# Optimization experiments

Hardware: AMD Instinct MI355X
Metric: run time of the kernel (lower is better)

## Reference

```python
import jax, jax.numpy as jnp
import numpy as np

N_NODES = 10000
N_EDGES = 100000
N_GRAPHS = 64
EMBED = 512
HIDDEN = 1024
N_LAYERS = 3
N_GAUSS = 50
RBF_RADIUS = 12.0
AVG_LEN = 60.0
CONNECTIVITY = 32.0


def setup_inputs() -> dict:
    key = jax.random.key(0)
    ks = jax.random.split(key, 20)
    x = jax.random.normal(ks[0], (N_NODES, EMBED), dtype=jnp.float32)
    edge_index = jax.random.randint(ks[1], (2, N_EDGES), 0, N_NODES, dtype=jnp.int32)
    batch = jnp.sort(jax.random.randint(ks[2], (N_NODES,), 0, N_GRAPHS, dtype=jnp.int32))
    dist = jax.random.uniform(ks[3], (N_EDGES,), dtype=jnp.float32) * RBF_RADIUS
    v = jax.random.normal(ks[4], (N_EDGES, 3), dtype=jnp.float32)
    vec_hat = v / (jnp.linalg.norm(v, axis=-1, keepdims=True) + 1e-12)

    def lin(k, fan_in, shape):
        bound = 1.0 / np.sqrt(fan_in)
        return jax.random.uniform(k, shape, jnp.float32, -bound, bound)

    in_dim = 3 * EMBED
    params = {
        'rbf_W': lin(ks[5], N_GAUSS, (N_GAUSS, EMBED)),
        'rbf_b': lin(ks[6], N_GAUSS, (EMBED,)),
        'e_Win': lin(ks[7], in_dim, (in_dim, HIDDEN)),
        'e_bin': lin(ks[8], in_dim, (HIDDEN,)),
        'e_Wh': lin(ks[9], HIDDEN, (N_LAYERS, HIDDEN, HIDDEN)),
        'e_bh': lin(ks[10], HIDDEN, (N_LAYERS, HIDDEN)),
        'e_Wout': lin(ks[11], HIDDEN, (HIDDEN, 1)),
        'e_bout': lin(ks[12], HIDDEN, (1,)),
        'f_Win': lin(ks[13], in_dim, (in_dim, HIDDEN)),
        'f_bin': lin(ks[14], in_dim, (HIDDEN,)),
        'f_Wh': lin(ks[15], HIDDEN, (N_LAYERS, HIDDEN, HIDDEN)),
        'f_bh': lin(ks[16], HIDDEN, (N_LAYERS, HIDDEN)),
        'f_Wout': lin(ks[17], HIDDEN, (HIDDEN, 1)),
        'f_bout': lin(ks[18], HIDDEN, (1,)),
    }
    return {'x': x, 'edge_index': edge_index, 'batch': batch, 'dist': dist,
            'vec_hat': vec_hat, **params}


def _rbf(dist, W, b):
    # Gaussian smearing over [0, rbf_radius] followed by linear embed
    offsets = jnp.linspace(0.0, RBF_RADIUS, N_GAUSS, dtype=jnp.float32)
    coeff = -0.5 / (offsets[1] - offsets[0]) ** 2
    gauss = jnp.exp(coeff * (dist[:, None] - offsets[None, :]) ** 2)  # [E, G]
    return gauss @ W + b  # [E, embed]


def _resmlp(h, Win, bin_, Wh, bh, Wout, bout):
    h = jax.nn.silu(h @ Win + bin_)
    for i in range(N_LAYERS):
        h = h + jax.nn.silu(h @ Wh[i] + bh[i])
    return h @ Wout + bout  # [E, 1]


def reference(x, edge_index, batch, dist, vec_hat,
              rbf_W, rbf_b,
              e_Win, e_bin, e_Wh, e_bh, e_Wout, e_bout,
              f_Win, f_bin, f_Wh, f_bh, f_Wout, f_bout):
    src, dst = edge_index[0], edge_index[1]
    rbf = _rbf(dist, rbf_W, rbf_b)  # [E, embed]
    inputs = jnp.concatenate([x[src], x[dst], rbf], axis=-1)  # [E, 3*embed]
    energy_pairs = _resmlp(inputs, e_Win, e_bin, e_Wh, e_bh, e_Wout, e_bout)  # [E,1]
    force_pairs = _resmlp(inputs, f_Win, f_bin, f_Wh, f_bh, f_Wout, f_bout) * vec_hat  # [E,3]
    energy = jax.ops.segment_sum(energy_pairs, batch[src], num_segments=N_GRAPHS)
    energy = energy / (AVG_LEN * CONNECTIVITY)  # [G,1]
    forces = jax.ops.segment_sum(force_pairs, src, num_segments=N_NODES) / CONNECTIVITY  # [N,3]
    return energy, forces
```

## Files before the change

kernel.cpp:

```cpp
#include <hip/hip_runtime.h>

#define E_EDGES 100000
#define E_PAD   100096
#define NNODES  10000
#define NPAD    10112
#define NGRAPHS 64

typedef __attribute__((ext_vector_type(4))) float f32x4;
typedef __attribute__((ext_vector_type(8))) short short8;

__device__ __forceinline__ unsigned short f2bf(float f) {
  union { float f; unsigned u; } v; v.f = f;
  unsigned u = v.u;
  return (unsigned short)((u + 0x7FFFu + ((u >> 16) & 1u)) >> 16);
}
__device__ __forceinline__ float bf2f(unsigned short h) {
  union { unsigned u; float f; } v; v.u = ((unsigned)h) << 16;
  return v.f;
}

struct TDesc { const float* src; unsigned short* dst; int R, C, srcLd, dstLd; };
struct TDescs { TDesc d[10]; };

__global__ __launch_bounds__(256) void transpose_all(TDescs ds) {
  TDesc t = ds.d[blockIdx.z];
  int x0 = blockIdx.x * 32, y0 = blockIdx.y * 32;
  if (x0 >= t.C || y0 >= t.R) return;
  __shared__ float tile[32][33];
  int tx = threadIdx.x & 31, ty = threadIdx.x >> 5;
#pragma unroll
  for (int i = 0; i < 4; ++i)
    tile[ty + i * 8][tx] = t.src[(size_t)(y0 + ty + i * 8) * t.srcLd + x0 + tx];
  __syncthreads();
#pragma unroll
  for (int i = 0; i < 4; ++i) {
    int c = ty + i * 8;
    t.dst[(size_t)(x0 + c) * t.dstLd + y0 + tx] = f2bf(tile[tx][c]);
  }
}

__global__ void mbuild_kernel(const float* __restrict__ rbf_W, const float* __restrict__ rbf_b,
                              const float* __restrict__ e_Win, const float* __restrict__ e_bin,
                              const float* __restrict__ f_Win, const float* __restrict__ f_bin,
                              unsigned short* __restrict__ M_t) {
  int gid = blockIdx.x * 256 + threadIdx.x;
  int n = gid >> 6, k = gid & 63;
  const float* Wp; float bn; int col;
  if (n < 1024) { Wp = e_Win + 1024 * 1024; col = n;        bn = e_bin[n]; }
  else          { Wp = f_Win + 1024 * 1024; col = n - 1024; bn = f_bin[n - 1024]; }
  float acc = 0.f;
  if (k < 50) {
    for (int i = 0; i < 512; ++i) acc += rbf_W[k * 512 + i] * Wp[(size_t)i * 1024 + col];
  } else if (k == 50) {
    for (int i = 0; i < 512; ++i) acc += rbf_b[i] * Wp[(size_t)i * 1024 + col];
    acc += bn;
  }
  M_t[n * 64 + k] = f2bf(acc);
}

__global__ void gauss_kernel(const float* __restrict__ dist, unsigned short* __restrict__ G) {
  int gid = blockIdx.x * 256 + threadIdx.x;
  if (gid >= E_PAD * 64) return;
  int e = gid >> 6, g = gid & 63;
  float val = 0.f;
  if (e < E_EDGES) {
    if (g < 50) {
      const float step = 12.0f / 49.0f;
      float d = dist[e] - step * (float)g;
      val = __expf((-0.5f / (step * step)) * d * d);
    } else if (g == 50) val = 1.0f;
  }
  G[gid] = f2bf(val);
}

__global__ void xconv_kernel(const float* __restrict__ x, unsigned short* __restrict__ xb) {
  int gid = blockIdx.x * 256 + threadIdx.x;
  int r = gid >> 9;
  xb[gid] = f2bf(r < NNODES ? x[gid] : 0.f);
}

template<int MODE>
__global__ __launch_bounds__(256, 3)
void gemm_kernel(const unsigned short* __restrict__ A, const unsigned short* __restrict__ Bt,
                 const float* __restrict__ bias, unsigned short* __restrict__ C,
                 const float* __restrict__ wout, float* __restrict__ pairs,
                 int K, int ldc, int nRows, int nColBlk) {
  __shared__ __align__(16) unsigned short As[128 * 64];
  __shared__ __align__(16) unsigned short Bs[128 * 64];
  const int nblk = gridDim.x;
  const int bid  = blockIdx.x;
  const int swz  = (bid & 7) * (nblk >> 3) + (bid >> 3);
  const int rowBlk = swz / nColBlk;
  const int colBlk = swz - rowBlk * nColBlk;
  const int rowBase = rowBlk * 128;
  const int colBase = colBlk * 128;
  const int tid  = threadIdx.x;
  const int wave = tid >> 6, lane = tid & 63;
  const int wr = wave >> 1, wc = wave & 1;
  const int lrow = lane & 15;
  const int lk   = (lane >> 4) << 3;
  const int r0 = (lane >> 4) << 2;
  const int c0 = lane & 15;
  const int ktRes = (colBase >> 6) + wc;

  f32x4 acc[4][4];
#pragma unroll
  for (int m = 0; m < 4; ++m)
#pragma unroll
    for (int n = 0; n < 4; ++n) acc[m][n] = (f32x4){0.f, 0.f, 0.f, 0.f};

  unsigned short resv[4][4][4];

  const int nk = K >> 6;
  for (int kt = 0; kt < nk; ++kt) {
    const int k0 = kt << 6;
    __syncthreads();
#pragma unroll
    for (int i = 0; i < 4; ++i) {
      int chunk = wave * 4 + i;
      int eoff  = (chunk * 64 + lane) * 8;
      int r = eoff >> 6, c = eoff & 63;
      const unsigned short* ga = A  + (size_t)(rowBase + r) * K + (k0 + c);
      const unsigned short* gb = Bt + (size_t)(colBase + r) * K + (k0 + c);
      __builtin_amdgcn_global_load_lds((const __attribute__((address_space(1))) void*)ga,
          (__attribute__((address_space(3))) void*)(As + chunk * 512), 16, 0, 0);
      __builtin_amdgcn_global_load_lds((const __attribute__((address_space(1))) void*)gb,
          (__attribute__((address_space(3))) void*)(Bs + chunk * 512), 16, 0, 0);
    }
    __syncthreads();
#pragma unroll
    for (int kk = 0; kk < 2; ++kk) {
      short8 a[4], b[4];
#pragma unroll
      for (int m = 0; m < 4; ++m)
        a[m] = *(const short8*)&As[(wr * 64 + m * 16 + lrow) * 64 + kk * 32 + lk];
#pragma unroll
      for (int n = 0; n < 4; ++n)
        b[n] = *(const short8*)&Bs[(wc * 64 + n * 16 + lrow) * 64 + kk * 32 + lk];
#pragma unroll
      for (int m = 0; m < 4; ++m)
#pragma unroll
        for (int n = 0; n < 4; ++n)
          acc[m][n] = __builtin_amdgcn_mfma_f32_16x16x32_bf16(a[m], b[n], acc[m][n], 0, 0, 0);
    }
    if (MODE >= 1 && kt == ktRes) {
#pragma unroll
      for (int m = 0; m < 4; ++m)
#pragma unroll
        for (int n = 0; n < 4; ++n)
#pragma unroll
          for (int j = 0; j < 4; ++j)
            resv[m][n][j] = As[(wr * 64 + m * 16 + r0 + j) * 64 + (n * 16 + c0)];
    }
  }

  float rsum[4][4];
  if (MODE == 2) {
#pragma unroll
    for (int m = 0; m < 4; ++m)
#pragma unroll
      for (int j = 0; j < 4; ++j) rsum[m][j] = 0.f;
  }

#pragma unroll
  for (int n = 0; n < 4; ++n) {
    int colg = colBase + wc * 64 + n * 16 + c0;
    float bv = (MODE >= 1) ? bias[colg] : 0.f;
    float wv = (MODE == 2) ? wout[colg] : 0.f;
#pragma unroll
    for (int m = 0; m < 4; ++m) {
      int rowg = rowBase + wr * 64 + m * 16 + r0;
#pragma unroll
      for (int j = 0; j < 4; ++j) {
        float v = acc[m][n][j] + bv;
        float s;
        if (MODE >= 1) s = v / (1.f + __expf(-v)) + bf2f(resv[m][n][j]);
        else           s = v;
        if (MODE == 2) rsum[m][j] += s * wv;
        else           C[(size_t)(rowg + j) * ldc + colg] = f2bf(s);
      }
    }
  }

  if (MODE == 2) {
#pragma unroll
    for (int m = 0; m < 4; ++m)
#pragma unroll
      for (int j = 0; j < 4; ++j) {
        float v = rsum[m][j];
        v += __shfl_xor(v, 1); v += __shfl_xor(v, 2);
        v += __shfl_xor(v, 4); v += __shfl_xor(v, 8);
        if (c0 == 0) {
          int rowg = rowBase + wr * 64 + m * 16 + r0 + j;
          if (rowg < nRows) atomicAdd(&pairs[rowg], v);
        }
      }
  }
}

__global__ __launch_bounds__(256, 3)
void fuse1_kernel(const unsigned short* __restrict__ G, const unsigned short* __restrict__ M_t,
                  const unsigned short* __restrict__ PS, const int* __restrict__ srcI,
                  const int* __restrict__ dstI, unsigned short* __restrict__ H,
                  int colOff, int e0) {
  __shared__ __align__(16) unsigned short Gs[128 * 64];
  __shared__ __align__(16) unsigned short Ms[128 * 64];
  __shared__ int sIdx[128], dIdx[128];
  const int rowBase = blockIdx.x * 128;
  const int nBase   = blockIdx.y * 128;
  const int tid  = threadIdx.x;
  const int wave = tid >> 6, lane = tid & 63;
  const int wr = wave >> 1, wc = wave & 1;
  const int lrow = lane & 15;
  const int lk   = (lane >> 4) << 3;

  {
    int r = tid & 127;
    int e = e0 + rowBase + r;
    if (tid < 128) sIdx[r] = (e < E_EDGES) ? srcI[e] : 0;
    else           dIdx[r] = (e < E_EDGES) ? dstI[e] : 0;
  }
#pragma unroll
  for (int i = 0; i < 4; ++i) {
    int chunk = wave * 4 + i;
    int eoff  = (chunk * 64 + lane) * 8;
    const unsigned short* gg = G   + (size_t)(e0 + rowBase) * 64 + eoff;
    const unsigned short* gm = M_t + (size_t)(colOff + nBase) * 64 + eoff;
    __builtin_amdgcn_global_load_lds((const __attribute__((address_space(1))) void*)gg,
        (__attribute__((address_space(3))) void*)(Gs + chunk * 512), 16, 0, 0);
    __builtin_amdgcn_global_load_lds((const __attribute__((address_space(1))) void*)gm,
        (__attribute__((address_space(3))) void*)(Ms + chunk * 512), 16, 0, 0);
  }
  __syncthreads();

  f32x4 acc[4][4];
#pragma unroll
  for (int m = 0; m < 4; ++m)
#pragma unroll
    for (int n = 0; n < 4; ++n) acc[m][n] = (f32x4){0.f, 0.f, 0.f, 0.f};
#pragma unroll
  for (int kk = 0; kk < 2; ++kk) {
    short8 a[4], b[4];
#pragma unroll
    for (int m = 0; m < 4; ++m)
      a[m] = *(const short8*)&Gs[(wr * 64 + m * 16 + lrow) * 64 + kk * 32 + lk];
#pragma unroll
    for (int n = 0; n < 4; ++n)
      b[n] = *(const short8*)&Ms[(wc * 64 + n * 16 + lrow) * 64 + kk * 32 + lk];
#pragma unroll
    for (int m = 0; m < 4; ++m)
#pragma unroll
      for (int n = 0; n < 4; ++n)
        acc[m][n] = __builtin_amdgcn_mfma_f32_16x16x32_bf16(a[m], b[n], acc[m][n], 0, 0, 0);
  }

  const int r0 = (lane >> 4) << 2;
  const int c0 = lane & 15;
#pragma unroll
  for (int m = 0; m < 4; ++m)
#pragma unroll
    for (int j = 0; j < 4; ++j) {
      int rowl = wr * 64 + m * 16 + r0 + j;
      int s = sIdx[rowl], d = dIdx[rowl];
      const unsigned short* prs = PS + (size_t)s * 4096 + 2 * colOff;
      const unsigned short* prd = PS + (size_t)d * 4096 + 2 * colOff + 1024;
#pragma unroll
      for (int n = 0; n < 4; ++n) {
        int nloc = nBase + wc * 64 + n * 16 + c0;
        float v = acc[m][n][j] + bf2f(prs[nloc]) + bf2f(prd[nloc]);
        H[(size_t)(rowBase + rowl) * 1024 + nloc] = f2bf(v / (1.f + __expf(-v)));
      }
    }
}

__global__ void init_kernel(float* __restrict__ pe, float* __restrict__ pf,
                            float* __restrict__ out, int outN,
                            const float* __restrict__ eb, const float* __restrict__ fb) {
  int i = blockIdx.x * 256 + threadIdx.x;
  if (i < E_EDGES) pe[i] = eb[0];
  else if (i < 2 * E_EDGES) pf[i - E_EDGES] = fb[0];
  else if (i < 2 * E_EDGES + outN) out[i - 2 * E_EDGES] = 0.f;
}

__global__ void energy_kernel(const float* __restrict__ pairs, const int* __restrict__ srcI,
                              const int* __restrict__ batch, float* __restrict__ out) {
  __shared__ float bins[NGRAPHS];
  if (threadIdx.x < NGRAPHS) bins[threadIdx.x] = 0.f;
  __syncthreads();
  for (int e = blockIdx.x * 256 + threadIdx.x; e < E_EDGES; e += gridDim.x * 256)
    atomicAdd(&bins[batch[srcI[e]]], pairs[e]);
  __syncthreads();
  if (threadIdx.x < NGRAPHS)
    atomicAdd(&out[threadIdx.x], bins[threadIdx.x] * (1.0f / 1920.0f));
}

__global__ void force_kernel(const float* __restrict__ pairs, const int* __restrict__ srcI,
                             const float* __restrict__ vec, float* __restrict__ out) {
  int e = blockIdx.x * 256 + threadIdx.x;
  if (e >= E_EDGES) return;
  float p = pairs[e] * (1.0f / 32.0f);
  int s = srcI[e];
  atomicAdd(&out[64 + s * 3 + 0], p * vec[e * 3 + 0]);
  atomicAdd(&out[64 + s * 3 + 1], p * vec[e * 3 + 1]);
  atomicAdd(&out[64 + s * 3 + 2], p * vec[e * 3 + 2]);
}

extern "C" void kernel_launch(void* const* d_in, const int* in_sizes, int n_in,
                              void* d_out, int out_size, void* d_ws, size_t ws_size,
                              hipStream_t stream) {
  const float* x       = (const float*)d_in[0];
  const int*   ei      = (const int*)  d_in[1];
  const int*   batch   = (const int*)  d_in[2];
  const float* dist    = (const float*)d_in[3];
  const float* vec_hat = (const float*)d_in[4];
  const float* rbf_W   = (const float*)d_in[5];
  const float* rbf_b   = (const float*)d_in[6];
  const float* e_Win   = (const float*)d_in[7];
  const float* e_bin   = (const float*)d_in[8];
  const float* e_Wh    = (const float*)d_in[9];
  const float* e_bh    = (const float*)d_in[10];
  const float* e_Wout  = (const float*)d_in[11];
  const float* e_bout  = (const float*)d_in[12];
  const float* f_Win   = (const float*)d_in[13];
  const float* f_bin   = (const float*)d_in[14];
  const float* f_Wh    = (const float*)d_in[15];
  const float* f_bh    = (const float*)d_in[16];
  const float* f_Wout  = (const float*)d_in[17];
  const float* f_bout  = (const float*)d_in[18];

  const int* srcI = ei;
  const int* dstI = ei + E_EDGES;

  size_t off = 0;
  char* base = (char*)d_ws;
  auto alloc = [&](size_t bytes) -> void* {
    void* p = base + off;
    off = (off + bytes + 255) & ~(size_t)255;
    return p;
  };
  unsigned short* WtN   = (unsigned short*)alloc((size_t)4096 * 512 * 2);
  unsigned short* Wt_eh = (unsigned short*)alloc((size_t)3 * 1024 * 1024 * 2);
  unsigned short* Wt_fh = (unsigned short*)alloc((size_t)3 * 1024 * 1024 * 2);
  unsigned short* M_t   = (unsigned short*)alloc((size_t)2048 * 64 * 2);
  unsigned short* xb    = (unsigned short*)alloc((size_t)NPAD * 512 * 2);
  unsigned short* G     = (unsigned short*)alloc((size_t)E_PAD * 64 * 2);
  unsigned short* PS    = (unsigned short*)alloc((size_t)NPAD * 4096 * 2);
  float* pairs_e = (float*)alloc((size_t)E_EDGES * 4);
  float* pairs_f = (float*)alloc((size_t)E_EDGES * 4);

  size_t avail = (ws_size > off + 4096) ? (ws_size - off - 4096) : 0;
  long long rows = (long long)(avail / 4096);
  int EC = (int)(rows - rows % 128);
  if (EC > E_PAD) EC = E_PAD;
  if (EC < 128) return;

  unsigned short* bufA = (unsigned short*)alloc((size_t)EC * 1024 * 2);
  unsigned short* bufC = (unsigned short*)alloc((size_t)EC * 1024 * 2);
  if (ws_size < off) return;

  init_kernel<<<(2 * E_EDGES + out_size + 255) / 256, 256, 0, stream>>>(
      pairs_e, pairs_f, (float*)d_out, out_size, e_bout, f_bout);

  TDescs td;
  td.d[0] = {e_Win,              WtN,               512, 1024, 1024, 512};
  td.d[1] = {e_Win + 512 * 1024, WtN + 1024 * 512,  512, 1024, 1024, 512};
  td.d[2] = {f_Win,              WtN + 2048 * 512,  512, 1024, 1024, 512};
  td.d[3] = {f_Win + 512 * 1024, WtN + 3072 * 512,  512, 1024, 1024, 512};
  for (int l = 0; l < 3; ++l) {
    td.d[4 + l] = {e_Wh + (size_t)l * 1048576, Wt_eh + (size_t)l * 1048576, 1024, 1024, 1024, 1024};
    td.d[7 + l] = {f_Wh + (size_t)l * 1048576, Wt_fh + (size_t)l * 1048576, 1024, 1024, 1024, 1024};
  }
  transpose_all<<<dim3(32, 32, 10), 256, 0, stream>>>(td);

  mbuild_kernel<<<(2048 * 64) / 256, 256, 0, stream>>>(rbf_W, rbf_b, e_Win, e_bin, f_Win, f_bin, M_t);
  gauss_kernel<<<(E_PAD * 64) / 256, 256, 0, stream>>>(dist, G);
  xconv_kernel<<<(NPAD * 512) / 256, 256, 0, stream>>>(x, xb);

  gemm_kernel<0><<<(NPAD / 128) * 32, 256, 0, stream>>>(
      xb, WtN, nullptr, PS, nullptr, nullptr, 512, 4096, NPAD, 32);

  for (int e0 = 0; e0 < E_EDGES; e0 += EC) {
    int rem = E_EDGES - e0; if (rem > EC) rem = EC;
    int rowsPad = ((rem + 127) / 128) * 128;
    int nblk = (rowsPad / 128) * 8;
    dim3 gf(rowsPad / 128, 8);

    fuse1_kernel<<<gf, 256, 0, stream>>>(G, M_t, PS, srcI, dstI, bufA, 0, e0);
    gemm_kernel<1><<<nblk, 256, 0, stream>>>(bufA, Wt_eh + (size_t)0 * 1048576, e_bh + 0,
                                             bufC, nullptr, nullptr, 1024, 1024, rowsPad, 8);
    gemm_kernel<1><<<nblk, 256, 0, stream>>>(bufC, Wt_eh + (size_t)1 * 1048576, e_bh + 1024,
                                             bufA, nullptr, nullptr, 1024, 1024, rowsPad, 8);
    gemm_kernel<2><<<nblk, 256, 0, stream>>>(bufA, Wt_eh + (size_t)2 * 1048576, e_bh + 2048,
                                             nullptr, e_Wout, pairs_e + e0, 1024, 1024, rem, 8);

    fuse1_kernel<<<gf, 256, 0, stream>>>(G, M_t, PS, srcI, dstI, bufC, 1024, e0);
    gemm_kernel<1><<<nblk, 256, 0, stream>>>(bufC, Wt_fh + (size_t)0 * 1048576, f_bh + 0,
                                             bufA, nullptr, nullptr, 1024, 1024, rowsPad, 8);
    gemm_kernel<1><<<nblk, 256, 0, stream>>>(bufA, Wt_fh + (size_t)1 * 1048576, f_bh + 1024,
                                             bufC, nullptr, nullptr, 1024, 1024, rowsPad, 8);
    gemm_kernel<2><<<nblk, 256, 0, stream>>>(bufC, Wt_fh + (size_t)2 * 1048576, f_bh + 2048,
                                             nullptr, f_Wout, pairs_f + e0, 1024, 1024, rem, 8);
  }

  energy_kernel<<<256, 256, 0, stream>>>(pairs_e, srcI, batch, (float*)d_out);
  force_kernel<<<(E_EDGES + 255) / 256, 256, 0, stream>>>(pairs_f, srcI, vec_hat, (float*)d_out);
}
```

Measured before the change: 2.225 ms.

## Replace hidden-layer GEMMs with 256x256 tile, double-buffered, 8-wave pipelined kernel

Adds a gemm8_kernel that computes 256x256 output tiles with 8 waves, a double-buffered 128KB LDS stage, an XOR swizzle against bank conflicts, interleaved global-to-LDS prefetch with split MFMA phases, s_setprio, and an XCD-aware block remap. The residual is now read from global memory in the epilogue instead of being captured from LDS. The old gemm kernel is reduced to the plain MODE 0 projection. The aim is more operand reuse per tile and overlap of loads with MFMA in the dominant 1024x1024 layers. In exchange it uses large LDS that limits occupancy, pads edges to 256 rows, and adds an extra global read for the residual.

```diff
diff --git a/kernel.cpp b/kernel.cpp
--- a/kernel.cpp
+++ b/kernel.cpp
@@ -101,15 +101,12 @@
   const int lk   = (lane >> 4) << 3;
   const int r0 = (lane >> 4) << 2;
   const int c0 = lane & 15;
-  const int ktRes = (colBase >> 6) + wc;
 
   f32x4 acc[4][4];
 #pragma unroll
   for (int m = 0; m < 4; ++m)
 #pragma unroll
     for (int n = 0; n < 4; ++n) acc[m][n] = (f32x4){0.f, 0.f, 0.f, 0.f};
-
-  unsigned short resv[4][4][4];
 
   const int nk = K >> 6;
   for (int kt = 0; kt < nk; ++kt) {
@@ -143,55 +140,178 @@
         for (int n = 0; n < 4; ++n)
           acc[m][n] = __builtin_amdgcn_mfma_f32_16x16x32_bf16(a[m], b[n], acc[m][n], 0, 0, 0);
     }
-    if (MODE >= 1 && kt == ktRes) {
-#pragma unroll
-      for (int m = 0; m < 4; ++m)
-#pragma unroll
-        for (int n = 0; n < 4; ++n)
-#pragma unroll
-          for (int j = 0; j < 4; ++j)
-            resv[m][n][j] = As[(wr * 64 + m * 16 + r0 + j) * 64 + (n * 16 + c0)];
-    }
-  }
-
-  float rsum[4][4];
-  if (MODE == 2) {
-#pragma unroll
-    for (int m = 0; m < 4; ++m)
-#pragma unroll
-      for (int j = 0; j < 4; ++j) rsum[m][j] = 0.f;
   }
 
 #pragma unroll
   for (int n = 0; n < 4; ++n) {
     int colg = colBase + wc * 64 + n * 16 + c0;
-    float bv = (MODE >= 1) ? bias[colg] : 0.f;
-    float wv = (MODE == 2) ? wout[colg] : 0.f;
 #pragma unroll
     for (int m = 0; m < 4; ++m) {
       int rowg = rowBase + wr * 64 + m * 16 + r0;
 #pragma unroll
+      for (int j = 0; j < 4; ++j)
+        C[(size_t)(rowg + j) * ldc + colg] = f2bf(acc[m][n][j]);
+    }
+  }
+}
+
+template<int MODE>
+__global__ __launch_bounds__(512, 2)
+void gemm8_kernel(const unsigned short* __restrict__ A, const unsigned short* __restrict__ Bt,
+                  const float* __restrict__ bias, unsigned short* __restrict__ C,
+                  const float* __restrict__ wout, float* __restrict__ pairs,
+                  int K, int nRows, int nColBlk) {
+  __shared__ __align__(16) char smem[131072];
+  const int nwg = gridDim.x, orig = blockIdx.x;
+  const int xcd = orig & 7, q = nwg >> 3, rr = nwg & 7;
+  const int wgid = (xcd < rr ? xcd * (q + 1) : rr * (q + 1) + (xcd - rr) * q) + (orig >> 3);
+  const int rowBlk = wgid / nColBlk;
+  const int colBlk = wgid - rowBlk * nColBlk;
+  const int rowBase = rowBlk * 256, colBase = colBlk * 256;
+  const int tid = threadIdx.x, w = tid >> 6, lane = tid & 63;
+  const int wr = w >> 2, wcn = w & 3;
+  const int lrow = lane & 15, hi = lane >> 4;
+  const int r0 = hi << 2, c0 = lane & 15;
+  const int nk = K >> 6;
+
+  auto stageHalf = [&](const unsigned short* gsrc, char* ldsBase) {
+#pragma unroll
+    for (int i = 0; i < 2; ++i) {
+      int r = i * 64 + w * 8 + (lane >> 3);
+      int cb = ((lane & 7) * 16) ^ (((r >> 2) & 1) << 6);
+      __builtin_amdgcn_global_load_lds(
+          (const __attribute__((address_space(1))) void*)(gsrc + (size_t)r * K + (cb >> 1)),
+          (__attribute__((address_space(3))) void*)(ldsBase + i * 8192 + w * 1024), 16, 0, 0);
+    }
+  };
+  auto stageA = [&](int t, int h) {
+    stageHalf(A + (size_t)(rowBase + h * 128) * K + t * 64, smem + (t & 1) * 65536 + h * 16384);
+  };
+  auto stageB = [&](int t, int h) {
+    stageHalf(Bt + (size_t)(colBase + h * 128) * K + t * 64,
+              smem + (t & 1) * 65536 + 32768 + h * 16384);
+  };
+  auto ldsA = [&](int c, int m, int ks) -> short8 {
+    const char* hb = smem + c * 65536 + wr * 16384;
+    int row = m * 16 + lrow;
+    int byte = ((row << 7) | (ks * 64 + hi * 16)) ^ (((row >> 2) & 1) << 6);
+    return *(const short8*)(hb + byte);
+  };
+  auto ldsB = [&](int c, int n, int ks) -> short8 {
+    const char* hb = smem + c * 65536 + 32768 + (wcn >> 1) * 16384;
+    int row = (wcn & 1) * 64 + n * 16 + lrow;
+    int byte = ((row << 7) | (ks * 64 + hi * 16)) ^ (((row >> 2) & 1) << 6);
+    return *(const short8*)(hb + byte);
+  };
+
+  f32x4 acc[8][4];
+#pragma unroll
+  for (int m = 0; m < 8; ++m)
+#pragma unroll
+    for (int n = 0; n < 4; ++n) acc[m][n] = (f32x4){0.f, 0.f, 0.f, 0.f};
+  short8 aF[8][2], bF[2][2];
+
+  stageA(0, 0); stageA(0, 1); stageB(0, 0); stageB(0, 1);
+  stageA(1, 0); stageA(1, 1);
+  asm volatile("s_waitcnt vmcnt(4)" ::: "memory");
+  asm volatile("s_barrier" ::: "memory");
+
+  for (int t = 0; t < nk; ++t) {
+    const int c = t & 1;
+    if (t + 1 < nk) stageB(t + 1, 0);
+#pragma unroll
+    for (int m = 0; m < 4; ++m) { aF[m][0] = ldsA(c, m, 0); aF[m][1] = ldsA(c, m, 1); }
+#pragma unroll
+    for (int n = 0; n < 2; ++n) { bF[n][0] = ldsB(c, n, 0); bF[n][1] = ldsB(c, n, 1); }
+    asm volatile("s_barrier" ::: "memory");
+    __builtin_amdgcn_s_setprio(1);
+#pragma unroll
+    for (int m = 0; m < 4; ++m)
+#pragma unroll
+      for (int n = 0; n < 2; ++n)
+#pragma unroll
+        for (int ks = 0; ks < 2; ++ks)
+          acc[m][n] = __builtin_amdgcn_mfma_f32_16x16x32_bf16(aF[m][ks], bF[n][ks], acc[m][n], 0, 0, 0);
+    __builtin_amdgcn_s_setprio(0);
+    asm volatile("s_barrier" ::: "memory");
+    if (t + 1 < nk) stageB(t + 1, 1);
+#pragma unroll
+    for (int m = 4; m < 8; ++m) { aF[m][0] = ldsA(c, m, 0); aF[m][1] = ldsA(c, m, 1); }
+    asm volatile("s_barrier" ::: "memory");
+    __builtin_amdgcn_s_setprio(1);
+#pragma unroll
+    for (int m = 4; m < 8; ++m)
+#pragma unroll
+      for (int n = 0; n < 2; ++n)
+#pragma unroll
+        for (int ks = 0; ks < 2; ++ks)
+          acc[m][n] = __builtin_amdgcn_mfma_f32_16x16x32_bf16(aF[m][ks], bF[n][ks], acc[m][n], 0, 0, 0);
+    __builtin_amdgcn_s_setprio(0);
+    asm volatile("s_barrier" ::: "memory");
+    if (t + 2 < nk) stageA(t + 2, 0);
+#pragma unroll
+    for (int n = 0; n < 2; ++n) { bF[n][0] = ldsB(c, n + 2, 0); bF[n][1] = ldsB(c, n + 2, 1); }
+    asm volatile("s_barrier" ::: "memory");
+    __builtin_amdgcn_s_setprio(1);
+#pragma unroll
+    for (int m = 4; m < 8; ++m)
+#pragma unroll
+      for (int n = 0; n < 2; ++n)
+#pragma unroll
+        for (int ks = 0; ks < 2; ++ks)
+          acc[m][n + 2] = __builtin_amdgcn_mfma_f32_16x16x32_bf16(aF[m][ks], bF[n][ks], acc[m][n + 2], 0, 0, 0);
+    __builtin_amdgcn_s_setprio(0);
+    asm volatile("s_barrier" ::: "memory");
+    if (t + 2 < nk) stageA(t + 2, 1);
+    asm volatile("s_barrier" ::: "memory");
+    __builtin_amdgcn_s_setprio(1);
+#pragma unroll
+    for (int m = 0; m < 4; ++m)
+#pragma unroll
+      for (int n = 0; n < 2; ++n)
+#pragma unroll
+        for (int ks = 0; ks < 2; ++ks)
+          acc[m][n + 2] = __builtin_amdgcn_mfma_f32_16x16x32_bf16(aF[m][ks], bF[n][ks], acc[m][n + 2], 0, 0, 0);
+    __builtin_amdgcn_s_setprio(0);
+    if (t + 2 < nk)      { asm volatile("s_waitcnt vmcnt(4)" ::: "memory"); }
+    else if (t + 1 < nk) { asm volatile("s_waitcnt vmcnt(0)" ::: "memory"); }
+    asm volatile("s_barrier" ::: "memory");
+  }
+
+  float rsum[8][4];
+  if (MODE == 2) {
+#pragma unroll
+    for (int m = 0; m < 8; ++m)
+#pragma unroll
+      for (int j = 0; j < 4; ++j) rsum[m][j] = 0.f;
+  }
+#pragma unroll
+  for (int n = 0; n < 4; ++n) {
+    int colg = colBase + wcn * 64 + n * 16 + c0;
+    float bv = bias[colg];
+    float wv = (MODE == 2) ? wout[colg] : 0.f;
+#pragma unroll
+    for (int m = 0; m < 8; ++m) {
+      int rowg = rowBase + wr * 128 + m * 16 + r0;
+#pragma unroll
       for (int j = 0; j < 4; ++j) {
         float v = acc[m][n][j] + bv;
-        float s;
-        if (MODE >= 1) s = v / (1.f + __expf(-v)) + bf2f(resv[m][n][j]);
-        else           s = v;
+        float s = v / (1.f + __expf(-v)) + bf2f(A[(size_t)(rowg + j) * K + colg]);
         if (MODE == 2) rsum[m][j] += s * wv;
-        else           C[(size_t)(rowg + j) * ldc + colg] = f2bf(s);
+        else           C[(size_t)(rowg + j) * 1024 + colg] = f2bf(s);
       }
     }
   }
-
   if (MODE == 2) {
 #pragma unroll
-    for (int m = 0; m < 4; ++m)
+    for (int m = 0; m < 8; ++m)
 #pragma unroll
       for (int j = 0; j < 4; ++j) {
         float v = rsum[m][j];
         v += __shfl_xor(v, 1); v += __shfl_xor(v, 2);
         v += __shfl_xor(v, 4); v += __shfl_xor(v, 8);
         if (c0 == 0) {
-          int rowg = rowBase + wr * 64 + m * 16 + r0 + j;
+          int rowg = rowBase + wr * 128 + m * 16 + r0 + j;
           if (rowg < nRows) atomicAdd(&pairs[rowg], v);
         }
       }
@@ -350,9 +470,9 @@
 
   size_t avail = (ws_size > off + 4096) ? (ws_size - off - 4096) : 0;
   long long rows = (long long)(avail / 4096);
-  int EC = (int)(rows - rows % 128);
+  int EC = (int)(rows - rows % 256);
   if (EC > E_PAD) EC = E_PAD;
-  if (EC < 128) return;
+  if (EC < 256) return;
 
   unsigned short* bufA = (unsigned short*)alloc((size_t)EC * 1024 * 2);
   unsigned short* bufC = (unsigned short*)alloc((size_t)EC * 1024 * 2);
@@ -381,25 +501,25 @@
 
   for (int e0 = 0; e0 < E_EDGES; e0 += EC) {
     int rem = E_EDGES - e0; if (rem > EC) rem = EC;
-    int rowsPad = ((rem + 127) / 128) * 128;
-    int nblk = (rowsPad / 128) * 8;
+    int rowsPad = ((rem + 255) / 256) * 256;
+    int nblk8 = (rowsPad / 256) * 4;
     dim3 gf(rowsPad / 128, 8);
 
     fuse1_kernel<<<gf, 256, 0, stream>>>(G, M_t, PS, srcI, dstI, bufA, 0, e0);
-    gemm_kernel<1><<<nblk, 256, 0, stream>>>(bufA, Wt_eh + (size_t)0 * 1048576, e_bh + 0,
-                                             bufC, nullptr, nullptr, 1024, 1024, rowsPad, 8);
-    gemm_kernel<1><<<nblk, 256, 0, stream>>>(bufC, Wt_eh + (size_t)1 * 1048576, e_bh + 1024,
-                                             bufA, nullptr, nullptr, 1024, 1024, rowsPad, 8);
-    gemm_kernel<2><<<nblk, 256, 0, stream>>>(bufA, Wt_eh + (size_t)2 * 1048576, e_bh + 2048,
-                                             nullptr, e_Wout, pairs_e + e0, 1024, 1024, rem, 8);
+    gemm8_kernel<1><<<nblk8, 512, 0, stream>>>(bufA, Wt_eh + (size_t)0 * 1048576, e_bh + 0,
+                                               bufC, nullptr, nullptr, 1024, rowsPad, 4);
+    gemm8_kernel<1><<<nblk8, 512, 0, stream>>>(bufC, Wt_eh + (size_t)1 * 1048576, e_bh + 1024,
+                                               bufA, nullptr, nullptr, 1024, rowsPad, 4);
+    gemm8_kernel<2><<<nblk8, 512, 0, stream>>>(bufA, Wt_eh + (size_t)2 * 1048576, e_bh + 2048,
+                                               nullptr, e_Wout, pairs_e + e0, 1024, rem, 4);
 
     fuse1_kernel<<<gf, 256, 0, stream>>>(G, M_t, PS, srcI, dstI, bufC, 1024, e0);
-    gemm_kernel<1><<<nblk, 256, 0, stream>>>(bufC, Wt_fh + (size_t)0 * 1048576, f_bh + 0,
-                                             bufA, nullptr, nullptr, 1024, 1024, rowsPad, 8);
-    gemm_kernel<1><<<nblk, 256, 0, stream>>>(bufA, Wt_fh + (size_t)1 * 1048576, f_bh + 1024,
-                                             bufC, nullptr, nullptr, 1024, 1024, rowsPad, 8);
-    gemm_kernel<2><<<nblk, 256, 0, stream>>>(bufC, Wt_fh + (size_t)2 * 1048576, f_bh + 2048,
-                                             nullptr, f_Wout, pairs_f + e0, 1024, 1024, rem, 8);
+    gemm8_kernel<1><<<nblk8, 512, 0, stream>>>(bufC, Wt_fh + (size_t)0 * 1048576, f_bh + 0,
+                                               bufA, nullptr, nullptr, 1024, rowsPad, 4);
+    gemm8_kernel<1><<<nblk8, 512, 0, stream>>>(bufA, Wt_fh + (size_t)1 * 1048576, f_bh + 1024,
+                                               bufC, nullptr, nullptr, 1024, rowsPad, 4);
+    gemm8_kernel<2><<<nblk8, 512, 0, stream>>>(bufC, Wt_fh + (size_t)2 * 1048576, f_bh + 2048,
+                                               nullptr, f_Wout, pairs_f + e0, 1024, rem, 4);
   }
 
   energy_kernel<<<256, 256, 0, stream>>>(pairs_e, srcI, batch, (float*)d_out);
```

Measured after the change: 3.267 ms. 1.47x slower.
